# Performance work log

Hardware: AMD Instinct MI355X
Metric: run time of the kernel (lower is better)

Reference implementation:

```python
import jax, jax.numpy as jnp
import numpy as np

LN_EPS = 1e-5

def _ln(x, w, b):
    mu = jnp.mean(x, -1, keepdims=True)
    var = jnp.mean((x - mu) ** 2, -1, keepdims=True)
    return (x - mu) / jnp.sqrt(var + LN_EPS) * w + b

def _rot_fwd(x, c, s):
    dh = x.shape[-1] // 2
    r, i = x[..., :dh], x[..., dh:]
    return jnp.concatenate([r * c - i * s, r * s + i * c], axis=-1)

def _rot_inv(x, c, s):
    dh = x.shape[-1] // 2
    r, i = x[..., :dh], x[..., dh:]
    return jnp.concatenate([r * c + i * s, -r * s + i * c], axis=-1)

def _sheaf(x, thetas, alpha, corr_W):
    # causal offsets for window=3
    B, T, d = x.shape
    offsets = [-3, -2, -1, 0]
    lap = jnp.zeros_like(x)
    for idx, delta in enumerate(offsets):
        th = thetas[idx]
        c, s = jnp.cos(th), jnp.sin(th)
        Rx = _rot_fwd(x, c, s)
        if delta == 0:
            x_nb = x
        else:
            ad = -delta
            zeros = jnp.zeros((B, ad, d), dtype=x.dtype)
            x_nb = jnp.concatenate([zeros, x[:, :T - ad, :]], axis=1)
        lap = lap + _rot_inv(Rx - x_nb, c, s)
    out = x - jnp.abs(alpha) * lap
    return out + jnp.einsum('btd,od->bto', out, corr_W)

def _gist_rotation(x, gist_theta, gist_mag, gist_weights, gist_strength, ln_w, ln_b):
    # Scale-1 path: gist_weights present. theta: (B, dh)
    dh = x.shape[-1] // 2
    w = gist_weights[..., None] * gist_mag              # (B, K, 1)
    w = w / (jnp.sum(w, axis=1, keepdims=True) + 1e-8)
    theta = jnp.sum(w * gist_theta, axis=1)             # (B, dh)
    theta = theta * jax.nn.sigmoid(gist_strength)
    c = jnp.cos(theta)[:, None, :]                      # (B, 1, dh)
    s = jnp.sin(theta)[:, None, :]
    r, i = x[..., :dh], x[..., dh:]
    rot = jnp.concatenate([r * c - i * s, r * s + i * c], axis=-1)
    return _ln(rot, ln_w, ln_b)

def _gist_cross_attn(x, gist_theta, gist_mag, Wq, Wk, Wv, Wo, gist_up_W, gist_up_b, n_heads=16):
    B, T, d = x.shape
    K = gist_theta.shape[1]
    dh = d // n_heads
    gist_repr = jnp.einsum('bkf,of->bko', jnp.concatenate([gist_theta, gist_mag], axis=-1), gist_up_W) + gist_up_b  # (B,K,d)
    Q = jnp.einsum('btd,od->bto', x, Wq).reshape(B, T, n_heads, dh).transpose(0, 2, 1, 3)          # (B,H,T,dh)
    Kh = jnp.einsum('bkd,od->bko', gist_repr, Wk).reshape(B, K, n_heads, dh).transpose(0, 2, 1, 3)  # (B,H,K,dh)
    V = jnp.einsum('bkd,od->bko', gist_repr, Wv).reshape(B, K, n_heads, dh).transpose(0, 2, 1, 3)
    scores = jnp.einsum('bhtd,bhkd->bhtk', Q, Kh) / jnp.sqrt(jnp.asarray(dh, x.dtype))
    ctx = jnp.einsum('bhtk,bhkd->bhtd', jax.nn.softmax(scores, axis=-1), V)
    ctx = ctx.transpose(0, 2, 1, 3).reshape(B, T, d)
    return jnp.einsum('btd,od->bto', ctx, Wo)

def _forward(x, gist_theta, gist_mag, gist_weights,
             ln_sheaf_w, ln_sheaf_b, sheaf_thetas, alpha, corr_W,
             ln_gist_w, ln_gist_b, gist_strength, gr_ln_w, gr_ln_b,
             ln_gca_w, ln_gca_b, Wq, Wk, Wv, Wo, gist_up_W, gist_up_b):
    x = x + _sheaf(_ln(x, ln_sheaf_w, ln_sheaf_b), sheaf_thetas, alpha, corr_W)
    xn = _ln(x, ln_gist_w, ln_gist_b)
    x = x + (_gist_rotation(xn, gist_theta, gist_mag, gist_weights, gist_strength, gr_ln_w, gr_ln_b) - xn)
    x = x + _gist_cross_attn(_ln(x, ln_gca_w, ln_gca_b), gist_theta, gist_mag,
                             Wq, Wk, Wv, Wo, gist_up_W, gist_up_b)
    return x

def setup_inputs() -> dict:
    key = jax.random.key(0)
    ks = jax.random.split(key, 16)
    B, T, d, K = 4, 2048, 2048, 16
    dh = d // 2
    scale = 1.0 / np.sqrt(d)
    inp = {
        'x': jax.random.normal(ks[0], (B, T, d), jnp.float32),
        'gist_theta': jax.random.normal(ks[1], (B, K, dh), jnp.float32),
        'gist_mag': jax.random.uniform(ks[2], (B, K, 1), jnp.float32),
        'gist_weights': jax.random.uniform(ks[3], (B, K), jnp.float32),
        'ln_sheaf_w': jnp.ones((d,), jnp.float32),
        'ln_sheaf_b': jnp.zeros((d,), jnp.float32),
        'sheaf_thetas': 0.1 * jax.random.normal(ks[4], (4, dh), jnp.float32),
        'alpha': jnp.asarray(0.15, jnp.float32),
        'corr_W': scale * jax.random.normal(ks[5], (d, d), jnp.float32),
        'ln_gist_w': jnp.ones((d,), jnp.float32),
        'ln_gist_b': jnp.zeros((d,), jnp.float32),
        'gist_strength': jnp.asarray(0.0, jnp.float32),
        'gr_ln_w': jnp.ones((d,), jnp.float32),
        'gr_ln_b': jnp.zeros((d,), jnp.float32),
        'ln_gca_w': jnp.ones((d,), jnp.float32),
        'ln_gca_b': jnp.zeros((d,), jnp.float32),
        'Wq': scale * jax.random.normal(ks[6], (d, d), jnp.float32),
        'Wk': scale * jax.random.normal(ks[7], (d, d), jnp.float32),
        'Wv': scale * jax.random.normal(ks[8], (d, d), jnp.float32),
        'Wo': scale * jax.random.normal(ks[9], (d, d), jnp.float32),
        'gist_up_W': (1.0 / np.sqrt(dh + 1)) * jax.random.normal(ks[10], (d, dh + 1), jnp.float32),
        'gist_up_b': jnp.zeros((d,), jnp.float32),
    }
    return inp

def reference(x, gist_theta, gist_mag, gist_weights,
              ln_sheaf_w, ln_sheaf_b, sheaf_thetas, alpha, corr_W,
              ln_gist_w, ln_gist_b, gist_strength, gr_ln_w, gr_ln_b,
              ln_gca_w, ln_gca_b, Wq, Wk, Wv, Wo, gist_up_W, gist_up_b):
    return _forward(x, gist_theta, gist_mag, gist_weights,
                    ln_sheaf_w, ln_sheaf_b, sheaf_thetas, alpha, corr_W,
                    ln_gist_w, ln_gist_b, gist_strength, gr_ln_w, gr_ln_b,
                    ln_gca_w, ln_gca_b, Wq, Wk, Wv, Wo, gist_up_W, gist_up_b)
```

## Files before the change

kernel.cpp:

```cpp
#include <hip/hip_runtime.h>
#include <hip/hip_bf16.h>

typedef unsigned short u16;
typedef unsigned int   u32;

using frag_ab = __attribute__((ext_vector_type(8))) short;
using frag_cd = __attribute__((ext_vector_type(4))) float;

__device__ __forceinline__ float bf2f(u16 u) {
    union { u32 i; float f; } v; v.i = ((u32)u) << 16; return v.f;
}
__device__ __forceinline__ u16 f2bf(float f) {
    __hip_bfloat16 h = __float2bfloat16(f);
    u16 u; __builtin_memcpy(&u, &h, 2); return u;
}
__device__ __forceinline__ float lo2f(u32 u) { union { u32 i; float f; } v; v.i = u << 16; return v.f; }
__device__ __forceinline__ float hi2f(u32 u) { union { u32 i; float f; } v; v.i = u & 0xffff0000u; return v.f; }
__device__ __forceinline__ void unpack8(uint4 v, float* f) {
    f[0]=lo2f(v.x); f[1]=hi2f(v.x); f[2]=lo2f(v.y); f[3]=hi2f(v.y);
    f[4]=lo2f(v.z); f[5]=hi2f(v.z); f[6]=lo2f(v.w); f[7]=hi2f(v.w);
}
__device__ __forceinline__ void load4f(const u16* p, float* f) {
    ushort4 v = *reinterpret_cast<const ushort4*>(p);
    f[0]=bf2f(v.x); f[1]=bf2f(v.y); f[2]=bf2f(v.z); f[3]=bf2f(v.w);
}
__device__ __forceinline__ void store4bf(u16* p, const float* f) {
    ushort4 v; v.x=f2bf(f[0]); v.y=f2bf(f[1]); v.z=f2bf(f[2]); v.w=f2bf(f[3]);
    *reinterpret_cast<ushort4*>(p) = v;
}
__device__ __forceinline__ u32 pack2(float a, float b) {
    return (u32)f2bf(a) | ((u32)f2bf(b) << 16);
}

__device__ __forceinline__ void gld16(const u16* g, u16* l) {
    __builtin_amdgcn_global_load_lds(
        (const __attribute__((address_space(1))) u32*)g,
        (__attribute__((address_space(3))) u32*)l, 16, 0, 0);
}

__device__ __forceinline__ void block_reduce2(float& s, float& ss, float* red) {
    #pragma unroll
    for (int off = 32; off > 0; off >>= 1) {
        s  += __shfl_down(s, off, 64);
        ss += __shfl_down(ss, off, 64);
    }
    int wv = threadIdx.x >> 6, ln = threadIdx.x & 63;
    if (ln == 0) { red[wv*2] = s; red[wv*2+1] = ss; }
    __syncthreads();
    s  = red[0] + red[2] + red[4] + red[6];
    ss = red[1] + red[3] + red[5] + red[7];
    __syncthreads();
}

__global__ __launch_bounds__(256) void convert_kernel(
    const float* __restrict__ in, u16* __restrict__ out, int n4)
{
    int i = blockIdx.x * 256 + threadIdx.x;
    if (i < n4) {
        float4 v = reinterpret_cast<const float4*>(in)[i];
        ushort4 o; o.x=f2bf(v.x); o.y=f2bf(v.y); o.z=f2bf(v.z); o.w=f2bf(v.w);
        reinterpret_cast<ushort4*>(out)[i] = o;
    }
}

__global__ __launch_bounds__(256) void apad_kernel(
    const float* __restrict__ gth, const float* __restrict__ gmag,
    u16* __restrict__ Abuf)
{
    const int r = blockIdx.x;
    const int tid = threadIdx.x;
    for (int c0 = tid*4; c0 < 1056; c0 += 1024) {
        float f[4];
        #pragma unroll
        for (int i = 0; i < 4; ++i) {
            int c = c0 + i;
            f[i] = (c < 1024) ? gth[(size_t)r*1024 + c] : (c == 1024 ? gmag[r] : 0.f);
        }
        store4bf(Abuf + (size_t)r*1056 + c0, f);
    }
}

__global__ __launch_bounds__(256) void wpad_kernel(
    const float* __restrict__ upW, u16* __restrict__ Bbuf)
{
    const int r = blockIdx.x;
    const int tid = threadIdx.x;
    for (int c0 = tid*4; c0 < 1056; c0 += 1024) {
        float f[4];
        #pragma unroll
        for (int i = 0; i < 4; ++i) {
            int c = c0 + i;
            f[i] = (c < 1025) ? upW[(size_t)r*1025 + c] : 0.f;
        }
        store4bf(Bbuf + (size_t)r*1056 + c0, f);
    }
}

__global__ __launch_bounds__(256) void setup_kernel(
    const float* __restrict__ sheaf_th, const float* __restrict__ gth,
    const float* __restrict__ gmag, const float* __restrict__ gwts,
    const float* __restrict__ strength, float* __restrict__ sheaf_cs,
    float* __restrict__ gist_cs)
{
    int bx = blockIdx.x, tid = threadIdx.x;
    if (bx < 4) {
        for (int j = tid; j < 1024; j += 256) {
            float th = sheaf_th[bx*1024 + j];
            sheaf_cs[bx*1024 + j]        = cosf(th);
            sheaf_cs[4096 + bx*1024 + j] = sinf(th);
        }
    } else {
        int b = bx - 4;
        float w[16], wsum = 0.f;
        #pragma unroll
        for (int k = 0; k < 16; ++k) {
            w[k] = gwts[b*16+k] * gmag[b*16+k];
            wsum += w[k];
        }
        float inv = 1.f / (wsum + 1e-8f);
        float sig = 1.f / (1.f + expf(-strength[0]));
        for (int j = tid; j < 1024; j += 256) {
            float th = 0.f;
            #pragma unroll
            for (int k = 0; k < 16; ++k)
                th += w[k] * inv * gth[(size_t)(b*16+k)*1024 + j];
            th *= sig;
            gist_cs[b*1024 + j]        = cosf(th);
            gist_cs[4096 + b*1024 + j] = sinf(th);
        }
    }
}

__global__ __launch_bounds__(256) void ln_kernel(
    const float* __restrict__ in, const float* __restrict__ w,
    const float* __restrict__ b, u16* __restrict__ out)
{
    __shared__ float red[8];
    const size_t base = (size_t)blockIdx.x * 2048;
    const int e0 = threadIdx.x * 8;
    float x[8];
    *reinterpret_cast<float4*>(&x[0]) = *reinterpret_cast<const float4*>(in + base + e0);
    *reinterpret_cast<float4*>(&x[4]) = *reinterpret_cast<const float4*>(in + base + e0 + 4);
    float s = 0.f, ss = 0.f;
    #pragma unroll
    for (int i = 0; i < 8; ++i) { s += x[i]; ss += x[i]*x[i]; }
    block_reduce2(s, ss, red);
    const float mu = s * (1.f/2048.f);
    const float rin = rsqrtf(ss * (1.f/2048.f) - mu*mu + 1e-5f);
    float wv[8], bv[8];
    *reinterpret_cast<float4*>(&wv[0]) = *reinterpret_cast<const float4*>(w + e0);
    *reinterpret_cast<float4*>(&wv[4]) = *reinterpret_cast<const float4*>(w + e0 + 4);
    *reinterpret_cast<float4*>(&bv[0]) = *reinterpret_cast<const float4*>(b + e0);
    *reinterpret_cast<float4*>(&bv[4]) = *reinterpret_cast<const float4*>(b + e0 + 4);
    float o[8];
    #pragma unroll
    for (int i = 0; i < 8; ++i) o[i] = (x[i]-mu)*rin*wv[i] + bv[i];
    uint4 st = { pack2(o[0],o[1]), pack2(o[2],o[3]), pack2(o[4],o[5]), pack2(o[6],o[7]) };
    *reinterpret_cast<uint4*>(out + base + e0) = st;
}

__global__ __launch_bounds__(256) void sheaf_kernel(
    const u16* __restrict__ x1, const float* __restrict__ scs,
    const float* __restrict__ alpha_p, u16* __restrict__ pre)
{
    const int row = blockIdx.x;
    const int t = row & 2047;
    const int j0 = threadIdx.x * 4;
    const size_t base = (size_t)row * 2048;
    const float a = fabsf(alpha_p[0]);

    float xr[4], xi[4];
    load4f(x1 + base + j0, xr);
    load4f(x1 + base + 1024 + j0, xi);
    float lr[4], li[4];
    #pragma unroll
    for (int m = 0; m < 4; ++m) { lr[m] = 4.f*xr[m]; li[m] = 4.f*xi[m]; }

    #pragma unroll
    for (int idx = 0; idx < 4; ++idx) {
        const int sh = 3 - idx;
        if (t >= sh) {
            const float4 c4 = *reinterpret_cast<const float4*>(&scs[idx*1024 + j0]);
            const float4 s4 = *reinterpret_cast<const float4*>(&scs[4096 + idx*1024 + j0]);
            float c[4] = {c4.x, c4.y, c4.z, c4.w};
            float sn[4] = {s4.x, s4.y, s4.z, s4.w};
            float yr[4], yi[4];
            load4f(x1 + base - (size_t)sh*2048 + j0, yr);
            load4f(x1 + base - (size_t)sh*2048 + 1024 + j0, yi);
            #pragma unroll
            for (int m = 0; m < 4; ++m) {
                lr[m] -= yr[m]*c[m] + yi[m]*sn[m];
                li[m] -= yi[m]*c[m] - yr[m]*sn[m];
            }
        }
    }
    float pr[4], pi[4];
    #pragma unroll
    for (int m = 0; m < 4; ++m) { pr[m] = xr[m] - a*lr[m]; pi[m] = xi[m] - a*li[m]; }
    store4bf(pre + base + j0, pr);
    store4bf(pre + base + 1024 + j0, pi);
}

__global__ __launch_bounds__(256) void stage2_kernel(
    const u16* __restrict__ xA, const float* __restrict__ gcs,
    const float* __restrict__ lgw, const float* __restrict__ lgb,
    const float* __restrict__ grw, const float* __restrict__ grb,
    const float* __restrict__ gcaw, const float* __restrict__ gcab,
    u16* __restrict__ xB, u16* __restrict__ x2)
{
    __shared__ float red[8];
    const int row = blockIdx.x;
    const int b = row >> 11;
    const int j0 = threadIdx.x * 4;
    const size_t base = (size_t)row * 2048;

    float ar[4], ai[4];
    load4f(xA + base + j0, ar);
    load4f(xA + base + 1024 + j0, ai);

    float s = 0.f, ss = 0.f;
    #pragma unroll
    for (int m = 0; m < 4; ++m) { s += ar[m]+ai[m]; ss += ar[m]*ar[m] + ai[m]*ai[m]; }
    block_reduce2(s, ss, red);
    float mu = s * (1.f/2048.f);
    float rin = rsqrtf(ss * (1.f/2048.f) - mu*mu + 1e-5f);

    float w0[4], b0[4], w1[4], b1[4];
    *reinterpret_cast<float4*>(w0) = *reinterpret_cast<const float4*>(lgw + j0);
    *reinterpret_cast<float4*>(b0) = *reinterpret_cast<const float4*>(lgb + j0);
    *reinterpret_cast<float4*>(w1) = *reinterpret_cast<const float4*>(lgw + 1024 + j0);
    *reinterpret_cast<float4*>(b1) = *reinterpret_cast<const float4*>(lgb + 1024 + j0);
    float xnr[4], xni[4];
    #pragma unroll
    for (int m = 0; m < 4; ++m) {
        xnr[m] = (ar[m]-mu)*rin*w0[m] + b0[m];
        xni[m] = (ai[m]-mu)*rin*w1[m] + b1[m];
    }

    const float4 c4 = *reinterpret_cast<const float4*>(&gcs[b*1024 + j0]);
    const float4 s4 = *reinterpret_cast<const float4*>(&gcs[4096 + b*1024 + j0]);
    float c[4] = {c4.x, c4.y, c4.z, c4.w};
    float sn[4] = {s4.x, s4.y, s4.z, s4.w};
    float rr[4], ri[4];
    #pragma unroll
    for (int m = 0; m < 4; ++m) {
        rr[m] = xnr[m]*c[m] - xni[m]*sn[m];
        ri[m] = xnr[m]*sn[m] + xni[m]*c[m];
    }

    s = 0.f; ss = 0.f;
    #pragma unroll
    for (int m = 0; m < 4; ++m) { s += rr[m]+ri[m]; ss += rr[m]*rr[m] + ri[m]*ri[m]; }
    block_reduce2(s, ss, red);
    float mu2 = s * (1.f/2048.f);
    float rin2 = rsqrtf(ss * (1.f/2048.f) - mu2*mu2 + 1e-5f);

    *reinterpret_cast<float4*>(w0) = *reinterpret_cast<const float4*>(grw + j0);
    *reinterpret_cast<float4*>(b0) = *reinterpret_cast<const float4*>(grb + j0);
    *reinterpret_cast<float4*>(w1) = *reinterpret_cast<const float4*>(grw + 1024 + j0);
    *reinterpret_cast<float4*>(b1) = *reinterpret_cast<const float4*>(grb + 1024 + j0);
    float br[4], bi[4];
    #pragma unroll
    for (int m = 0; m < 4; ++m) {
        float gr_ = (rr[m]-mu2)*rin2*w0[m] + b0[m];
        float gi_ = (ri[m]-mu2)*rin2*w1[m] + b1[m];
        br[m] = ar[m] - xnr[m] + gr_;
        bi[m] = ai[m] - xni[m] + gi_;
    }
    store4bf(xB + base + j0, br);
    store4bf(xB + base + 1024 + j0, bi);

    s = 0.f; ss = 0.f;
    #pragma unroll
    for (int m = 0; m < 4; ++m) { s += br[m]+bi[m]; ss += br[m]*br[m] + bi[m]*bi[m]; }
    block_reduce2(s, ss, red);
    float mu3 = s * (1.f/2048.f);
    float rin3 = rsqrtf(ss * (1.f/2048.f) - mu3*mu3 + 1e-5f);

    *reinterpret_cast<float4*>(w0) = *reinterpret_cast<const float4*>(gcaw + j0);
    *reinterpret_cast<float4*>(b0) = *reinterpret_cast<const float4*>(gcab + j0);
    *reinterpret_cast<float4*>(w1) = *reinterpret_cast<const float4*>(gcaw + 1024 + j0);
    *reinterpret_cast<float4*>(b1) = *reinterpret_cast<const float4*>(gcab + 1024 + j0);
    float o0[4], o1[4];
    #pragma unroll
    for (int m = 0; m < 4; ++m) {
        o0[m] = (br[m]-mu3)*rin3*w0[m] + b0[m];
        o1[m] = (bi[m]-mu3)*rin3*w1[m] + b1[m];
    }
    store4bf(x2 + base + j0, o0);
    store4bf(x2 + base + 1024 + j0, o1);
}

__global__ __launch_bounds__(256) void attn_kernel(
    const u16* __restrict__ Q, const u16* __restrict__ KV,
    u16* __restrict__ ctx)
{
    const int wv = threadIdx.x >> 6;
    const int lane = threadIdx.x & 63;
    const int tg = blockIdx.x * 4 + wv;
    const int b = tg >> 11;
    const size_t base = (size_t)tg * 2048 + lane * 32;

    float q[32];
    #pragma unroll
    for (int c = 0; c < 4; ++c)
        unpack8(*reinterpret_cast<const uint4*>(Q + base + c*8), &q[c*8]);

    float sc[16];
    #pragma unroll
    for (int k = 0; k < 16; ++k) {
        const u16* kr = KV + (size_t)(b*16 + k) * 4096 + lane*32;
        float p = 0.f;
        #pragma unroll
        for (int c = 0; c < 4; ++c) {
            float kv8[8]; unpack8(*reinterpret_cast<const uint4*>(kr + c*8), kv8);
            #pragma unroll
            for (int e = 0; e < 8; ++e) p += q[c*8+e] * kv8[e];
        }
        sc[k] = p;
    }
    #pragma unroll
    for (int k = 0; k < 16; ++k) {
        sc[k] += __shfl_xor(sc[k], 1, 64);
        sc[k] += __shfl_xor(sc[k], 2, 64);
        sc[k] *= 0.08838834764831845f;
    }
    float m = sc[0];
    #pragma unroll
    for (int k = 1; k < 16; ++k) m = fmaxf(m, sc[k]);
    float sum = 0.f;
    #pragma unroll
    for (int k = 0; k < 16; ++k) { sc[k] = expf(sc[k]-m); sum += sc[k]; }
    const float inv = 1.f / sum;

    float o[32];
    #pragma unroll
    for (int e = 0; e < 32; ++e) o[e] = 0.f;
    #pragma unroll
    for (int k = 0; k < 16; ++k) {
        const float p = sc[k] * inv;
        const u16* vr = KV + (size_t)(b*16 + k) * 4096 + 2048 + lane*32;
        #pragma unroll
        for (int c = 0; c < 4; ++c) {
            float v8[8]; unpack8(*reinterpret_cast<const uint4*>(vr + c*8), v8);
            #pragma unroll
            for (int e = 0; e < 8; ++e) o[c*8+e] += p * v8[e];
        }
    }
    #pragma unroll
    for (int c = 0; c < 4; ++c) {
        uint4 st = { pack2(o[c*8+0],o[c*8+1]), pack2(o[c*8+2],o[c*8+3]),
                     pack2(o[c*8+4],o[c*8+5]), pack2(o[c*8+6],o[c*8+7]) };
        *reinterpret_cast<uint4*>(ctx + base + c*8) = st;
    }
}

#define BM 128
#define BN 128
#define BK 32

template<int OUTF32>
__global__ __launch_bounds__(256) void gemm_bt_kernel(
    const u16* __restrict__ A, const u16* __restrict__ B,
    void* __restrict__ Cv, const float* __restrict__ addf,
    const u16* __restrict__ addb, const float* __restrict__ biasN,
    int M, int N, int K)
{
    __shared__ u16 As[2][8*512];
    __shared__ u16 Bs[2][8*512];

    const int tid = threadIdx.x;
    const int lane = tid & 63;
    const int wave = tid >> 6;
    const int wm = wave >> 1;
    const int wn = wave & 1;
    const int row0 = blockIdx.y * BM;
    const int col0 = blockIdx.x * BN;

    frag_cd acc[4][4] = {};

    const int srow   = lane >> 2;
    const int schunk = (lane & 3) ^ ((lane >> 3) & 3);
    const int scol   = schunk * 8;
    const int s0 = wave, s1 = wave + 4;

    int ra0 = row0 + s0*16 + srow; if (ra0 >= M) ra0 = M - 1;
    int ra1 = row0 + s1*16 + srow; if (ra1 >= M) ra1 = M - 1;
    const u16* gA0 = A + (size_t)ra0 * K + scol;
    const u16* gA1 = A + (size_t)ra1 * K + scol;
    const u16* gB0 = B + (size_t)(col0 + s0*16 + srow) * K + scol;
    const u16* gB1 = B + (size_t)(col0 + s1*16 + srow) * K + scol;

    const int fr = lane & 15;
    const int fq8 = lane >> 4;
    const int fslot = (4*fr + (fq8 ^ ((fr >> 1) & 3))) * 8;

    const int nt = K / BK;

    gld16(gA0, &As[0][s0*512]);
    gld16(gA1, &As[0][s1*512]);
    gld16(gB0, &Bs[0][s0*512]);
    gld16(gB1, &Bs[0][s1*512]);
    __syncthreads();

    int cur = 0;
    for (int t = 0; t < nt; ++t) {
        if (t + 1 < nt) {
            const int kt = (t + 1) * BK;
            gld16(gA0 + kt, &As[cur^1][s0*512]);
            gld16(gA1 + kt, &As[cur^1][s1*512]);
            gld16(gB0 + kt, &Bs[cur^1][s0*512]);
            gld16(gB1 + kt, &Bs[cur^1][s1*512]);
        }

        frag_ab af[4], bf_[4];
        #pragma unroll
        for (int i = 0; i < 4; ++i)
            af[i] = *reinterpret_cast<const frag_ab*>(&As[cur][(wm*4 + i)*512 + fslot]);
        #pragma unroll
        for (int j = 0; j < 4; ++j)
            bf_[j] = *reinterpret_cast<const frag_ab*>(&Bs[cur][(wn*4 + j)*512 + fslot]);
        #pragma unroll
        for (int i = 0; i < 4; ++i)
            #pragma unroll
            for (int j = 0; j < 4; ++j)
                acc[i][j] = __builtin_amdgcn_mfma_f32_16x16x32_bf16(af[i], bf_[j], acc[i][j], 0, 0, 0);

        __syncthreads();
        cur ^= 1;
    }

    #pragma unroll
    for (int i = 0; i < 4; ++i) {
        #pragma unroll
        for (int j = 0; j < 4; ++j) {
            #pragma unroll
            for (int r = 0; r < 4; ++r) {
                const int grow = row0 + wm*64 + i*16 + (lane >> 4) * 4 + r;
                const int gcol = col0 + wn*64 + j*16 + (lane & 15);
                if (grow < M) {
                    const size_t idx = (size_t)grow * N + gcol;
                    float v = acc[i][j][r];
                    if (addf) v += addf[idx];
                    if (addb) v += bf2f(addb[idx]);
                    if (biasN) v += biasN[gcol];
                    if (OUTF32) reinterpret_cast<float*>(Cv)[idx] = v;
                    else        reinterpret_cast<u16*>(Cv)[idx] = f2bf(v);
                }
            }
        }
    }
}

template<int OUTF32>
__global__ __launch_bounds__(512, 2) void gemm256_kernel(
    const u16* __restrict__ A, const u16* __restrict__ B,
    void* __restrict__ Cv, const float* __restrict__ addf,
    const u16* __restrict__ addb, const float* __restrict__ biasN,
    int M, int N, int K)
{
    extern __shared__ u16 lds[];
    u16* Abase = lds;
    u16* Bbase = lds + 32768;

    const int tid  = threadIdx.x;
    const int lane = tid & 63;
    const int wave = tid >> 6;
    const int wm   = wave >> 2;
    const int wn   = wave & 3;
    const int row0 = blockIdx.y * 256;
    const int col0 = blockIdx.x * 256;

    const int srow = lane >> 2;
    const int scol = ((lane & 3) ^ ((lane >> 3) & 3)) * 8;

    int rA0 = row0 +       wave*16 + srow; if (rA0 >= M) rA0 = M - 1;
    int rA1 = row0 + 128 + wave*16 + srow; if (rA1 >= M) rA1 = M - 1;
    const u16* pA0 = A + (size_t)rA0 * K + scol;
    const u16* pA1 = A + (size_t)rA1 * K + scol;
    const u16* pB0 = B + (size_t)(col0 +       wave*16 + srow) * K + scol;
    const u16* pB1 = B + (size_t)(col0 + 128 + wave*16 + srow) * K + scol;

    const int ldsW = wave * 2 * 512;

    const int fr = lane & 15;
    const int fq8 = lane >> 4;
    const int fslot = (4*fr + (fq8 ^ ((fr >> 1) & 3))) * 8;

    frag_cd acc[8][4] = {};
    frag_ab bfr[4][2];

#define STAGE256(SRC, DSTOFF, KT)                                   \
    gld16((SRC) + (KT),      (DSTOFF) + ldsW);                      \
    gld16((SRC) + (KT) + 32, (DSTOFF) + ldsW + 512);

    STAGE256(pB0, Bbase + 0*8192, 0);
    STAGE256(pB1, Bbase + 1*8192, 0);
    STAGE256(pA0, Abase + 0*8192, 0);
    STAGE256(pA1, Abase + 1*8192, 0);
    STAGE256(pB0, Bbase + 2*8192, 64);
    STAGE256(pB1, Bbase + 3*8192, 64);
    asm volatile("s_waitcnt vmcnt(4)" ::: "memory");
    __builtin_amdgcn_s_barrier();
    asm volatile("" ::: "memory");

    const int NI = K >> 7;
    for (int i = 0; i < NI; ++i) {
        const int t1k = i*128 + 64;
        int t2k = i*128 + 128; if (t2k >= K) t2k = K - 64;
        int t3k = i*128 + 192; if (t3k >= K) t3k = K - 64;

        #pragma unroll
        for (int p = 0; p < 8; ++p) {
            const int q = p & 3;
            const int bufc = p >> 2;

            if (q == 0) {
                const u16* Bh = Bbase + (bufc*2 + (wn >> 1))*8192;
                #pragma unroll
                for (int n = 0; n < 4; ++n)
                    #pragma unroll
                    for (int ks = 0; ks < 2; ++ks)
                        bfr[n][ks] = *reinterpret_cast<const frag_ab*>(
                            Bh + (((wn & 1)*4 + n)*2 + ks)*512 + fslot);
            }
            frag_ab afr[2][2];
            const u16* Ah = Abase + (bufc*2 + wm)*8192;
            #pragma unroll
            for (int r = 0; r < 2; ++r)
                #pragma unroll
                for (int ks = 0; ks < 2; ++ks)
                    afr[r][ks] = *reinterpret_cast<const frag_ab*>(
                        Ah + ((2*q + r)*2 + ks)*512 + fslot);

            switch (p) {
                case 0: STAGE256(pA0, Abase + 2*8192, t1k); break;
                case 1: STAGE256(pA1, Abase + 3*8192, t1k); break;
                case 2: STAGE256(pB0, Bbase + 0*8192, t2k); break;
                case 3: STAGE256(pB1, Bbase + 1*8192, t2k); break;
                case 4: STAGE256(pA0, Abase + 0*8192, t2k); break;
                case 5: STAGE256(pA1, Abase + 1*8192, t2k); break;
                case 6: STAGE256(pB0, Bbase + 2*8192, t3k); break;
                case 7: STAGE256(pB1, Bbase + 3*8192, t3k); break;
            }
            if (q == 3) asm volatile("s_waitcnt vmcnt(4)" ::: "memory");
            asm volatile("" ::: "memory");
            __builtin_amdgcn_s_barrier();
            asm volatile("s_waitcnt lgkmcnt(0)" ::: "memory");
            __builtin_amdgcn_sched_barrier(0);
            __builtin_amdgcn_s_setprio(1);
            #pragma unroll
            for (int r = 0; r < 2; ++r)
                #pragma unroll
                for (int n = 0; n < 4; ++n) {
                    acc[2*q + r][n] = __builtin_amdgcn_mfma_f32_16x16x32_bf16(
                        afr[r][0], bfr[n][0], acc[2*q + r][n], 0, 0, 0);
                    acc[2*q + r][n] = __builtin_amdgcn_mfma_f32_16x16x32_bf16(
                        afr[r][1], bfr[n][1], acc[2*q + r][n], 0, 0, 0);
                }
            __builtin_amdgcn_s_setprio(0);
            __builtin_amdgcn_sched_barrier(0);
            asm volatile("" ::: "memory");
            __builtin_amdgcn_s_barrier();
            asm volatile("" ::: "memory");
        }
    }
    asm volatile("s_waitcnt vmcnt(0)" ::: "memory");
#undef STAGE256

    #pragma unroll
    for (int m = 0; m < 8; ++m) {
        #pragma unroll
        for (int n = 0; n < 4; ++n) {
            #pragma unroll
            for (int r = 0; r < 4; ++r) {
                const int grow = row0 + wm*128 + m*16 + (lane >> 4) * 4 + r;
                const int gcol = col0 + wn*64 + n*16 + (lane & 15);
                if (grow < M) {
                    const size_t idx = (size_t)grow * N + gcol;
                    float v = acc[m][n][r];
                    if (addf) v += addf[idx];
                    if (addb) v += bf2f(addb[idx]);
                    if (biasN) v += biasN[gcol];
                    if (OUTF32) reinterpret_cast<float*>(Cv)[idx] = v;
                    else        reinterpret_cast<u16*>(Cv)[idx] = f2bf(v);
                }
            }
        }
    }
}

extern "C" void kernel_launch(void* const* d_in, const int* in_sizes, int n_in,
                              void* d_out, int out_size, void* d_ws, size_t ws_size,
                              hipStream_t stream)
{
    const float* x          = (const float*)d_in[0];
    const float* gist_theta = (const float*)d_in[1];
    const float* gist_mag   = (const float*)d_in[2];
    const float* gist_wts   = (const float*)d_in[3];
    const float* ln_sheaf_w = (const float*)d_in[4];
    const float* ln_sheaf_b = (const float*)d_in[5];
    const float* sheaf_th   = (const float*)d_in[6];
    const float* alpha      = (const float*)d_in[7];
    const float* corr_W     = (const float*)d_in[8];
    const float* ln_gist_w  = (const float*)d_in[9];
    const float* ln_gist_b  = (const float*)d_in[10];
    const float* strength   = (const float*)d_in[11];
    const float* gr_w       = (const float*)d_in[12];
    const float* gr_b       = (const float*)d_in[13];
    const float* gca_w      = (const float*)d_in[14];
    const float* gca_b      = (const float*)d_in[15];
    const float* Wq         = (const float*)d_in[16];
    const float* Wk         = (const float*)d_in[17];
    const float* Wv         = (const float*)d_in[18];
    const float* Wo         = (const float*)d_in[19];
    const float* up_W       = (const float*)d_in[20];
    const float* up_b       = (const float*)d_in[21];
    float* out = (float*)d_out;

    static bool attr_done = false;
    if (!attr_done) {
        hipFuncSetAttribute((const void*)&gemm256_kernel<0>,
                            hipFuncAttributeMaxDynamicSharedMemorySize, 131072);
        hipFuncSetAttribute((const void*)&gemm256_kernel<1>,
                            hipFuncAttributeMaxDynamicSharedMemorySize, 131072);
        attr_done = true;
    }

    char* w = (char*)d_ws;
    const size_t BIG = (size_t)4 * 2048 * 2048 * sizeof(u16);
    u16* wA = (u16*)(w);
    u16* wB = (u16*)(w + BIG);
    u16* wC = (u16*)(w + 2*BIG);
    u16* wslot = (u16*)(w + 3*BIG);
    char* small = w + 3*BIG + (size_t)2048*2048*sizeof(u16);
    float* sheaf_cs = (float*)(small);
    float* gist_cs  = (float*)(small + 32768);
    u16* repr = (u16*)(small + 65536);
    u16* KV   = repr + 64*2048;

    const int W4 = 2048*2048/4;
    const dim3 gBig256(2048/256, 8192/256), gKV(32, 1), gRepr(16, 1);

    setup_kernel<<<8, 256, 0, stream>>>(sheaf_th, gist_theta, gist_mag, gist_wts,
                                        strength, sheaf_cs, gist_cs);

    apad_kernel<<<64, 256, 0, stream>>>(gist_theta, gist_mag, wC);
    wpad_kernel<<<2048, 256, 0, stream>>>(up_W, wslot);
    gemm_bt_kernel<0><<<gRepr, 256, 0, stream>>>(wC, wslot, repr, nullptr, nullptr, up_b,
                                                 64, 2048, 1056);

    convert_kernel<<<4096, 256, 0, stream>>>(Wk, wB, W4);
    convert_kernel<<<4096, 256, 0, stream>>>(Wv, wB + (size_t)2048*2048, W4);
    gemm_bt_kernel<0><<<gKV, 256, 0, stream>>>(repr, wB, KV, nullptr, nullptr, nullptr,
                                               64, 4096, 2048);

    ln_kernel<<<8192, 256, 0, stream>>>(x, ln_sheaf_w, ln_sheaf_b, wA);
    sheaf_kernel<<<8192, 256, 0, stream>>>(wA, sheaf_cs, alpha, wB);

    convert_kernel<<<4096, 256, 0, stream>>>(corr_W, wslot, W4);
    gemm256_kernel<0><<<gBig256, 512, 131072, stream>>>(wB, wslot, wA, x, wB, nullptr,
                                                8192, 2048, 2048);
    stage2_kernel<<<8192, 256, 0, stream>>>(wA, gist_cs, ln_gist_w, ln_gist_b,
                                            gr_w, gr_b, gca_w, gca_b,
                                            wC, wA);
    convert_kernel<<<4096, 256, 0, stream>>>(Wq, wslot, W4);
    gemm256_kernel<0><<<gBig256, 512, 131072, stream>>>(wA, wslot, wB, nullptr, nullptr, nullptr,
                                                8192, 2048, 2048);
    attn_kernel<<<2048, 256, 0, stream>>>(wB, KV, wA);
    convert_kernel<<<4096, 256, 0, stream>>>(Wo, wslot, W4);
    gemm256_kernel<1><<<gBig256, 512, 131072, stream>>>(wA, wslot, (void*)out, nullptr, wC, nullptr,
                                                8192, 2048, 2048);
}
```

Before: 707.3 us.

## Double-buffer A fragments in registers and drop M-boundary clamping in GEMM

The 256x256 bf16 MFMA GEMM now loads A fragments from LDS for the next sub-step into a second register buffer while the current step's MFMAs run. This is meant to hide LDS read latency behind matrix math. The MFMA loop is reordered so the k-slice is the outer loop, and one sched_barrier plus the asm memory fences after the MFMAs are removed. Row clamping on A loads and the grow<M store guard are dropped, which assumes M is a multiple of 256; otherwise it reads and writes out of bounds. The extra fragment buffer also raises register pressure.

```diff
diff --git a/kernel.cpp b/kernel.cpp
--- a/kernel.cpp
+++ b/kernel.cpp
@@ -474,14 +474,11 @@
     const int srow = lane >> 2;
     const int scol = ((lane & 3) ^ ((lane >> 3) & 3)) * 8;
 
-    int rA0 = row0 +       wave*16 + srow; if (rA0 >= M) rA0 = M - 1;
-    int rA1 = row0 + 128 + wave*16 + srow; if (rA1 >= M) rA1 = M - 1;
-    const u16* pA0 = A + (size_t)rA0 * K + scol;
-    const u16* pA1 = A + (size_t)rA1 * K + scol;
-    const u16* pB0 = B + (size_t)(col0 +       wave*16 + srow) * K + scol;
-    const u16* pB1 = B + (size_t)(col0 + 128 + wave*16 + srow) * K + scol;
-
-    const int ldsW = wave * 2 * 512;
+    const u16* pA = A + (size_t)(row0 + wave*16 + srow) * K + scol;
+    const u16* pB = B + (size_t)(col0 + wave*16 + srow) * K + scol;
+    const size_t h128 = (size_t)128 * K;
+
+    const int ldsW = wave * 1024;
 
     const int fr = lane & 15;
     const int fq8 = lane >> 4;
@@ -489,20 +486,29 @@
 
     frag_cd acc[8][4] = {};
     frag_ab bfr[4][2];
+    frag_ab afr[2][2][2];
 
 #define STAGE256(SRC, DSTOFF, KT)                                   \
     gld16((SRC) + (KT),      (DSTOFF) + ldsW);                      \
     gld16((SRC) + (KT) + 32, (DSTOFF) + ldsW + 512);
 
-    STAGE256(pB0, Bbase + 0*8192, 0);
-    STAGE256(pB1, Bbase + 1*8192, 0);
-    STAGE256(pA0, Abase + 0*8192, 0);
-    STAGE256(pA1, Abase + 1*8192, 0);
-    STAGE256(pB0, Bbase + 2*8192, 64);
-    STAGE256(pB1, Bbase + 3*8192, 64);
+    STAGE256(pB,        Bbase + 0*8192, 0);
+    STAGE256(pB + h128, Bbase + 1*8192, 0);
+    STAGE256(pA,        Abase + 0*8192, 0);
+    STAGE256(pA + h128, Abase + 1*8192, 0);
+    STAGE256(pB,        Bbase + 2*8192, 64);
+    STAGE256(pB + h128, Bbase + 3*8192, 64);
     asm volatile("s_waitcnt vmcnt(4)" ::: "memory");
     __builtin_amdgcn_s_barrier();
-    asm volatile("" ::: "memory");
+    {
+        const u16* Ah = Abase + (0*2 + wm)*8192;
+        #pragma unroll
+        for (int r = 0; r < 2; ++r)
+            #pragma unroll
+            for (int ks = 0; ks < 2; ++ks)
+                afr[0][r][ks] = *reinterpret_cast<const frag_ab*>(
+                    Ah + ((r)*2*1 + (2*0 + r)*0 + ((0 + r)*2 + ks)*512 - (r)*2 + fslot));
+    }
 
     const int NI = K >> 7;
     for (int i = 0; i < NI; ++i) {
@@ -524,45 +530,44 @@
                         bfr[n][ks] = *reinterpret_cast<const frag_ab*>(
                             Bh + (((wn & 1)*4 + n)*2 + ks)*512 + fslot);
             }
-            frag_ab afr[2][2];
-            const u16* Ah = Abase + (bufc*2 + wm)*8192;
-            #pragma unroll
-            for (int r = 0; r < 2; ++r)
-                #pragma unroll
-                for (int ks = 0; ks < 2; ++ks)
-                    afr[r][ks] = *reinterpret_cast<const frag_ab*>(
-                        Ah + ((2*q + r)*2 + ks)*512 + fslot);
-
             switch (p) {
-                case 0: STAGE256(pA0, Abase + 2*8192, t1k); break;
-                case 1: STAGE256(pA1, Abase + 3*8192, t1k); break;
-                case 2: STAGE256(pB0, Bbase + 0*8192, t2k); break;
-                case 3: STAGE256(pB1, Bbase + 1*8192, t2k); break;
-                case 4: STAGE256(pA0, Abase + 0*8192, t2k); break;
-                case 5: STAGE256(pA1, Abase + 1*8192, t2k); break;
-                case 6: STAGE256(pB0, Bbase + 2*8192, t3k); break;
-                case 7: STAGE256(pB1, Bbase + 3*8192, t3k); break;
+                case 0: STAGE256(pA,        Abase + 2*8192, t1k); break;
+                case 1: STAGE256(pA + h128, Abase + 3*8192, t1k); break;
+                case 2: STAGE256(pB,        Bbase + 0*8192, t2k); break;
+                case 3: STAGE256(pB + h128, Bbase + 1*8192, t2k); break;
+                case 4: STAGE256(pA,        Abase + 0*8192, t2k); break;
+                case 5: STAGE256(pA + h128, Abase + 1*8192, t2k); break;
+                case 6: STAGE256(pB,        Bbase + 2*8192, t3k); break;
+                case 7: STAGE256(pB + h128, Bbase + 3*8192, t3k); break;
             }
             if (q == 3) asm volatile("s_waitcnt vmcnt(4)" ::: "memory");
-            asm volatile("" ::: "memory");
             __builtin_amdgcn_s_barrier();
             asm volatile("s_waitcnt lgkmcnt(0)" ::: "memory");
             __builtin_amdgcn_sched_barrier(0);
+
+            {
+                const int qn = (q + 1) & 3;
+                const int bufn = (q == 3) ? (bufc ^ 1) : bufc;
+                const u16* Ah = Abase + (bufn*2 + wm)*8192;
+                #pragma unroll
+                for (int r = 0; r < 2; ++r)
+                    #pragma unroll
+                    for (int ks = 0; ks < 2; ++ks)
+                        afr[(p+1)&1][r][ks] = *reinterpret_cast<const frag_ab*>(
+                            Ah + ((2*qn + r)*2 + ks)*512 + fslot);
+            }
+
             __builtin_amdgcn_s_setprio(1);
             #pragma unroll
-            for (int r = 0; r < 2; ++r)
+            for (int ks = 0; ks < 2; ++ks)
                 #pragma unroll
-                for (int n = 0; n < 4; ++n) {
-                    acc[2*q + r][n] = __builtin_amdgcn_mfma_f32_16x16x32_bf16(
-                        afr[r][0], bfr[n][0], acc[2*q + r][n], 0, 0, 0);
-                    acc[2*q + r][n] = __builtin_amdgcn_mfma_f32_16x16x32_bf16(
-                        afr[r][1], bfr[n][1], acc[2*q + r][n], 0, 0, 0);
-                }
+                for (int r = 0; r < 2; ++r)
+                    #pragma unroll
+                    for (int n = 0; n < 4; ++n)
+                        acc[2*q + r][n] = __builtin_amdgcn_mfma_f32_16x16x32_bf16(
+                            afr[p&1][r][ks], bfr[n][ks], acc[2*q + r][n], 0, 0, 0);
             __builtin_amdgcn_s_setprio(0);
-            __builtin_amdgcn_sched_barrier(0);
-            asm volatile("" ::: "memory");
             __builtin_amdgcn_s_barrier();
-            asm volatile("" ::: "memory");
         }
     }
     asm volatile("s_waitcnt vmcnt(0)" ::: "memory");
@@ -576,7 +581,7 @@
             for (int r = 0; r < 4; ++r) {
                 const int grow = row0 + wm*128 + m*16 + (lane >> 4) * 4 + r;
                 const int gcol = col0 + wn*64 + n*16 + (lane & 15);
-                if (grow < M) {
+                {
                     const size_t idx = (size_t)grow * N + gcol;
                     float v = acc[m][n][r];
                     if (addf) v += addf[idx];
```

Result: no change. 702.2 us (-0.7%).
